# Optimization experiments

Hardware: AMD Instinct MI355X
Metric: run time of the kernel (lower is better)

The kernel has to match this reference:

```python
import jax, jax.numpy as jnp
import numpy as np

N, E, C, H, G = 100000, 1600000, 128, 64, 512
TOL = 1e-7          # PyG topk tolerance
MIN_SCORE = 0.05
EPS_KL = 1e-14


def setup_inputs() -> dict:
    key = jax.random.key(0)
    ks = jax.random.split(key, 12)
    d = {}
    d["x"] = jax.random.normal(ks[0], (N, C), jnp.float32)
    d["edge_index"] = jax.random.randint(ks[1], (2, E), 0, N)
    d["batch"] = jnp.sort(jax.random.randint(ks[2], (N,), 0, G))
    d["attn"] = jax.random.uniform(ks[3], (N,), jnp.float32, minval=1e-3, maxval=1.0)
    def lin(k, i, o):
        return (jax.random.normal(k, (i, o), jnp.float32) / np.sqrt(i)).astype(jnp.float32)
    d["W1"] = lin(ks[4], C, H); d["b1"] = jnp.zeros((H,), jnp.float32)
    d["W2"] = lin(ks[5], H, H); d["b2"] = jnp.zeros((H,), jnp.float32)
    d["pool_w"] = (jax.random.normal(ks[6], (C,), jnp.float32) / np.sqrt(C)).astype(jnp.float32)
    d["W3"] = lin(ks[7], H, H); d["b3"] = jnp.zeros((H,), jnp.float32)
    d["W4"] = lin(ks[8], H, H); d["b4"] = jnp.zeros((H,), jnp.float32)
    d["Wl"] = lin(ks[9], H, 1); d["bl"] = jnp.zeros((1,), jnp.float32)
    return d


def _gin(x, src, dst, Wa, ba, Wb, bb, edge_w=None):
    # GINConv with eps=0: nn((1+0)*x + sum_{j in N(i)} x_j), nn = Lin-ReLU-Lin
    msg = x[src]                                   # [E, F] gather
    if edge_w is not None:
        msg = msg * edge_w[:, None]                # drop pruned edges
    agg = jax.ops.segment_sum(msg, dst, num_segments=x.shape[0])
    h = x + agg
    return jax.nn.relu(h @ Wa + ba) @ Wb + bb


def reference(x, edge_index, batch, attn, W1, b1, W2, b2, pool_w, W3, b3, W4, b4, Wl, bl):
    src, dst = edge_index[0], edge_index[1]
    out = jax.nn.relu(_gin(x, src, dst, W1, b1, W2, b2))

    # --- TopKPooling(min_score=0.05), attn=x ---
    raw = x @ pool_w                               # [N] attention logits
    m = jax.ops.segment_max(raw, batch, num_segments=G)
    e = jnp.exp(raw - m[batch])
    z = jax.ops.segment_sum(e, batch, num_segments=G)
    score = e / z[batch]                           # per-graph softmax
    smax = jax.ops.segment_max(score, batch, num_segments=G)
    thresh = jnp.minimum(smax[batch] - TOL, MIN_SCORE)
    mask = score > thresh                          # kept nodes (>=1 per graph)
    maskf = mask.astype(x.dtype)
    out = out * (score * maskf)[:, None]           # x[perm] * score[perm]
    edge_keep = maskf[src] * maskf[dst]            # filter_adj: both endpoints kept

    out = jax.nn.relu(_gin(out, src, dst, W3, b3, W4, b4, edge_w=edge_keep)) * maskf[:, None]
    graph_out = jax.ops.segment_sum(out, batch, num_segments=G)  # global_add_pool
    pred = (graph_out @ Wl + bl).reshape(-1)       # [G]

    # attn_loss = scatter_mean(kl_div(log(score+eps), attn[perm]), batch)
    kl = attn * (jnp.log(attn) - jnp.log(score + EPS_KL))
    cnt = jax.ops.segment_sum(maskf, batch, num_segments=G)
    attn_loss = jax.ops.segment_sum(kl * maskf, batch, num_segments=G) / jnp.maximum(cnt, 1.0)

    ratio = maskf.sum() / x.shape[0]
    return pred, attn_loss, ratio
```

## Files before the change

### kernel.cpp

```cpp
#include <hip/hip_runtime.h>
#include <math.h>

#define N_NODES 100000
#define N_EDGES 1600000
#define C_IN    128
#define H_DIM   64
#define G_GRAPHS 512
#define MAXG    4096
#define ELCAP   65536
#define KPG     32
#define NBITS   3136

__device__ __forceinline__ int lbound(const int* __restrict__ b, int val) {
    int lo = 0, hi = N_NODES;
    while (lo < hi) {
        int mid = (lo + hi) >> 1;
        if (b[mid] < val) lo = mid + 1; else hi = mid;
    }
    return lo;
}

__global__ void kpre(const float* __restrict__ x, const float* __restrict__ pool_w,
                     float* __restrict__ sc, unsigned int* __restrict__ zero_region) {
    int gid = blockIdx.x * blockDim.x + threadIdx.x;
    if (gid < NBITS + 1) zero_region[gid] = 0u;
    const int lane = threadIdx.x & 63;
    const int l32  = lane & 31;
    const int half = lane >> 5;
    const float4 pwv = ((const float4*)pool_w)[l32];
    const int wid = blockIdx.x * (blockDim.x >> 6) + (threadIdx.x >> 6);
    const int nw  = gridDim.x * (blockDim.x >> 6);
    for (int r0 = wid * 4; r0 < N_NODES; r0 += nw * 4) {
        int rowA = r0 + half;
        int rowB = r0 + 2 + half;
        float4 xa = ((const float4*)(x + (size_t)rowA * C_IN))[l32];
        float4 xb = ((const float4*)(x + (size_t)rowB * C_IN))[l32];
        float pa = xa.x * pwv.x + xa.y * pwv.y + xa.z * pwv.z + xa.w * pwv.w;
        float pb = xb.x * pwv.x + xb.y * pwv.y + xb.z * pwv.z + xb.w * pwv.w;
        #pragma unroll
        for (int m = 16; m > 0; m >>= 1) {
            pa += __shfl_xor(pa, m, 64);
            pb += __shfl_xor(pb, m, 64);
        }
        if (l32 == 0) { sc[rowA] = pa; sc[rowB] = pb; }
    }
}

__device__ __forceinline__ float blk_max(float v, float* red, int lane, int w) {
    #pragma unroll
    for (int m = 32; m > 0; m >>= 1) v = fmaxf(v, __shfl_xor(v, m, 64));
    if (lane == 0) red[w] = v;
    __syncthreads();
    float r = fmaxf(fmaxf(red[0], red[1]), fmaxf(red[2], red[3]));
    __syncthreads();
    return r;
}
__device__ __forceinline__ float blk_sum(float v, float* red, int lane, int w) {
    #pragma unroll
    for (int m = 32; m > 0; m >>= 1) v += __shfl_xor(v, m, 64);
    if (lane == 0) red[w] = v;
    __syncthreads();
    float r = (red[0] + red[1]) + (red[2] + red[3]);
    __syncthreads();
    return r;
}

__global__ void kA4(const int* __restrict__ batch, const float* __restrict__ attn,
                    float* __restrict__ sc, unsigned int* __restrict__ kept_bits,
                    int* __restrict__ klist, int* __restrict__ kcnt,
                    float* __restrict__ B, float* __restrict__ out) {
    __shared__ float buf[MAXG];
    __shared__ float red[4];
    __shared__ int   lst[KPG];
    __shared__ int   cntk;
    const int g = blockIdx.x;
    const int t = threadIdx.x;
    const int lane = t & 63;
    const int w = t >> 6;
    const int ns = lbound(batch, g);
    const int ne = lbound(batch, g + 1);
    const int cn = ne - ns;
    if (cn <= 0) {
        if (t == 0) { out[G_GRAPHS + g] = 0.f; kcnt[g] = 0; }
        return;
    }
    if (t == 0) cntk = 0;
    float lmax = -3.4e38f;
    for (int i = t; i < cn; i += 256) { float r = sc[ns + i]; buf[i] = r; lmax = fmaxf(lmax, r); }
    float m = blk_max(lmax, red, lane, w);
    float lsum = 0.f;
    for (int i = t; i < cn; i += 256) { float e = expf(buf[i] - m); buf[i] = e; lsum += e; }
    float z = blk_sum(lsum, red, lane, w);
    float thresh = fminf(1.f / z - 1e-7f, 0.05f);
    float klacc = 0.f;
    for (int i = t; i < cn; i += 256) {
        float s = buf[i] / z;
        if (s > thresh) {
            int n = ns + i;
            int p = atomicAdd(&cntk, 1);
            if (p < KPG) lst[p] = i;
            sc[n] = s;
            float a = attn[n];
            klacc += a * (logf(a) - logf(s + 1e-14f));
        }
    }
    float klsum = blk_sum(klacc, red, lane, w);
    int kct = cntk;
    int kc = kct < KPG ? kct : KPG;
    if (t == 0) {
        out[G_GRAPHS + g] = (kct > 0) ? klsum / (float)kct : 0.f;
        kcnt[g] = kc;
    }
    for (int i = t; i < kc; i += 256) {
        int n = ns + lst[i];
        klist[g * KPG + i] = n;
        atomicOr(&kept_bits[n >> 5], 1u << (n & 31));
    }
    for (int j = t; j < kc * H_DIM; j += 256)
        B[(size_t)(ns + lst[j >> 6]) * H_DIM + (j & 63)] = 0.f;
}

__device__ __forceinline__ void emit(bool hit, int s, int d, int* __restrict__ list,
                                     int cap, int* __restrict__ count, int lane) {
    unsigned long long bal = __ballot(hit);
    if (bal == 0ull) return;
    int leader = __ffsll((long long)bal) - 1;
    int cnt = __popcll(bal);
    int base = 0;
    if (lane == leader) base = atomicAdd(count, cnt);
    base = __shfl(base, leader, 64);
    if (hit) {
        int p = base + __popcll(bal & ((1ull << lane) - 1ull));
        if (p < cap) { list[p] = s; list[cap + p] = d; }
    }
}

__global__ void k5f2(const int* __restrict__ ei, const unsigned int* __restrict__ bits,
                     const float* __restrict__ x, const float* __restrict__ W1,
                     float* __restrict__ B, int* __restrict__ elsd,
                     int* __restrict__ elcount) {
    __shared__ float W1s[C_IN * H_DIM];
    __shared__ int ls[1024], ld[1024];
    __shared__ int c1;
    const int t = threadIdx.x;
    const int lane = t & 63;
    if (t == 0) c1 = 0;
    int t4 = blockIdx.x * 256 + t;
    bool valid = t4 < (N_EDGES / 4);
    int4 s4 = make_int4(0, 0, 0, 0), d4 = make_int4(0, 0, 0, 0);
    if (valid) {
        s4 = ((const int4*)ei)[t4];
        d4 = ((const int4*)(ei + N_EDGES))[t4];
    }
    __syncthreads();
    int sv[4] = {s4.x, s4.y, s4.z, s4.w};
    int dv[4] = {d4.x, d4.y, d4.z, d4.w};
    bool bk[4];
    #pragma unroll
    for (int q = 0; q < 4; ++q) {
        int ss = sv[q], dd = dv[q];
        bool kd = valid && (((bits[dd >> 5] >> (dd & 31)) & 1u) != 0u);
        bk[q] = kd && (((bits[ss >> 5] >> (ss & 31)) & 1u) != 0u);
        if (kd) { int p = atomicAdd(&c1, 1); ls[p] = ss; ld[p] = dd; }
    }
    #pragma unroll
    for (int q = 0; q < 4; ++q) emit(bk[q], sv[q], dv[q], elsd, ELCAP, elcount, lane);
    __syncthreads();
    const int nloc = c1;
    if (nloc == 0) return;
    for (int i = t; i < C_IN * H_DIM; i += 256) W1s[i] = W1[i];
    __syncthreads();
    const int w = t >> 6;
    for (int idx = w; idx < nloc; idx += 4) {
        int s = ls[idx];
        int d = ld[idx];
        const float4* xr = (const float4*)(x + (size_t)s * C_IN);
        float acc = 0.f;
        #pragma unroll 8
        for (int k4 = 0; k4 < C_IN / 4; ++k4) {
            float4 xv = xr[k4];
            acc = fmaf(xv.x, W1s[(4 * k4 + 0) * H_DIM + lane], acc);
            acc = fmaf(xv.y, W1s[(4 * k4 + 1) * H_DIM + lane], acc);
            acc = fmaf(xv.z, W1s[(4 * k4 + 2) * H_DIM + lane], acc);
            acc = fmaf(xv.w, W1s[(4 * k4 + 3) * H_DIM + lane], acc);
        }
        atomicAdd(&B[(size_t)d * H_DIM + lane], acc);
    }
}

__device__ __forceinline__ float computeA(int n, int lane,
                                          const float* __restrict__ x,
                                          const float* __restrict__ B,
                                          const float* __restrict__ sc,
                                          const float* __restrict__ W1, float b1l,
                                          const float* __restrict__ W2, float b2l,
                                          const float* __restrict__ W3) {
    const float4* xr = (const float4*)(x + (size_t)n * C_IN);
    float u = 0.f;
    #pragma unroll 8
    for (int k4 = 0; k4 < C_IN / 4; ++k4) {
        float4 xv = xr[k4];
        u = fmaf(xv.x, W1[(4 * k4 + 0) * H_DIM + lane], u);
        u = fmaf(xv.y, W1[(4 * k4 + 1) * H_DIM + lane], u);
        u = fmaf(xv.z, W1[(4 * k4 + 2) * H_DIM + lane], u);
        u = fmaf(xv.w, W1[(4 * k4 + 3) * H_DIM + lane], u);
    }
    float t1 = fmaxf(u + B[(size_t)n * H_DIM + lane] + b1l, 0.f);
    float o1 = b2l;
    #pragma unroll 8
    for (int k = 0; k < H_DIM; ++k) o1 = fmaf(__shfl(t1, k, 64), W2[k * H_DIM + lane], o1);
    o1 = fmaxf(o1, 0.f);
    float v = 0.f;
    #pragma unroll 8
    for (int k = 0; k < H_DIM; ++k) v = fmaf(__shfl(o1, k, 64), W3[k * H_DIM + lane], v);
    return v * sc[n];
}

__global__ void k8c(const int* __restrict__ klist, const int* __restrict__ kcnt,
                    const float* __restrict__ sc, const float* __restrict__ x,
                    const float* __restrict__ W1, const float* __restrict__ b1,
                    const float* __restrict__ W2, const float* __restrict__ b2,
                    const float* __restrict__ W3, const float* __restrict__ b3,
                    const float* __restrict__ W4, const float* __restrict__ b4,
                    const float* __restrict__ Wl, const float* __restrict__ bl,
                    const float* __restrict__ B, const int* __restrict__ elsd,
                    const int* __restrict__ elcount, float* __restrict__ out) {
    const int g = blockIdx.x;
    const int lane = threadIdx.x;
    const float b1l = b1[lane], b2l = b2[lane], b3l = b3[lane], b4l = b4[lane];
    const int kc = kcnt[g];
    int ec = *elcount; if (ec > ELCAP) ec = ELCAP;
    float gsum = 0.f;
    for (int i = 0; i < kc; ++i) {
        int n = __builtin_amdgcn_readfirstlane(klist[g * KPG + i]);
        float agg = 0.f;
        for (int base = 0; base < ec; base += 64) {
            int idx = base + lane;
            int dd = (idx < ec) ? elsd[ELCAP + idx] : -1;
            bool mtc = (dd == n);
            int ssl = mtc ? elsd[idx] : 0;
            unsigned long long bal = __ballot(mtc);
            while (bal) {
                int j = __ffsll((long long)bal) - 1;
                bal &= bal - 1;
                int s = __builtin_amdgcn_readfirstlane(__shfl(ssl, j, 64));
                agg += computeA(s, lane, x, B, sc, W1, b1l, W2, b2l, W3);
            }
        }
        float vA = computeA(n, lane, x, B, sc, W1, b1l, W2, b2l, W3);
        float t = fmaxf(vA + agg + b3l, 0.f);
        float o2 = b4l;
        #pragma unroll 8
        for (int k = 0; k < H_DIM; ++k) o2 = fmaf(__shfl(t, k, 64), W4[k * H_DIM + lane], o2);
        gsum += fmaxf(o2, 0.f);
    }
    float p = gsum * Wl[lane];
    #pragma unroll
    for (int m = 32; m > 0; m >>= 1) p += __shfl_xor(p, m, 64);
    if (lane == 0) out[g] = p + bl[0];
    if (g == 0) {
        int tot = 0;
        for (int i = lane; i < G_GRAPHS; i += 64) tot += kcnt[i];
        #pragma unroll
        for (int m = 32; m > 0; m >>= 1) tot += __shfl_xor(tot, m, 64);
        if (lane == 0) out[2 * G_GRAPHS] = (float)tot * (1.f / (float)N_NODES);
    }
}

extern "C" void kernel_launch(void* const* d_in, const int* in_sizes, int n_in,
                              void* d_out, int out_size, void* d_ws, size_t ws_size,
                              hipStream_t stream) {
    const float* x      = (const float*)d_in[0];
    const int*   ei     = (const int*)d_in[1];
    const int*   batch  = (const int*)d_in[2];
    const float* attn   = (const float*)d_in[3];
    const float* W1     = (const float*)d_in[4];
    const float* b1     = (const float*)d_in[5];
    const float* W2     = (const float*)d_in[6];
    const float* b2     = (const float*)d_in[7];
    const float* pool_w = (const float*)d_in[8];
    const float* W3     = (const float*)d_in[9];
    const float* b3     = (const float*)d_in[10];
    const float* W4     = (const float*)d_in[11];
    const float* b4     = (const float*)d_in[12];
    const float* Wl     = (const float*)d_in[13];
    const float* bl     = (const float*)d_in[14];
    float* out = (float*)d_out;

    float* B      = (float*)d_ws;
    float* sc     = B + (size_t)N_NODES * H_DIM;
    int*   klist  = (int*)(sc + N_NODES);
    int*   kcnt   = klist + G_GRAPHS * KPG;
    int*   elsd   = kcnt + G_GRAPHS;
    unsigned int* kept_bits = (unsigned int*)(elsd + 2 * ELCAP);
    int*          elcount   = (int*)(kept_bits + NBITS);

    kpre <<<2048, 256, 0, stream>>>(x, pool_w, sc, kept_bits);
    kA4  <<<G_GRAPHS, 256, 0, stream>>>(batch, attn, sc, kept_bits, klist, kcnt, B, out);
    k5f2 <<<(N_EDGES / 4 + 255) / 256, 256, 0, stream>>>(ei, kept_bits, x, W1, B,
                                                         elsd, elcount);
    k8c  <<<G_GRAPHS, 64, 0, stream>>>(klist, kcnt, sc, x, W1, b1, W2, b2, W3, b3,
                                       W4, b4, Wl, bl, B, elsd, elcount, out);
}
```

Baseline: 172.5 us.

## Precompute per-node first-GIN output once and precompute graph offsets

The final kernel used to recompute the first GIN layer output for every in-edge source, once per destination node, and it rescanned the edge list once per kept node. This change adds a kernel that computes that output once per kept node and stores it in B. The final kernel then scans the edge list a single time per graph, matching destinations against the kept list and accumulating into shared memory. Graph start offsets are now built in the pre-pass instead of by per-block binary search, and the W1 shared-memory staging in the edge-scan kernel is replaced by direct global reads. The cost is one extra kernel launch and an overwrite of B that depends on kAcomp running after kscan.

```diff
diff --git a/kernel.cpp b/kernel.cpp
--- a/kernel.cpp
+++ b/kernel.cpp
@@ -11,19 +11,22 @@
 #define KPG     32
 #define NBITS   3136
 
-__device__ __forceinline__ int lbound(const int* __restrict__ b, int val) {
-    int lo = 0, hi = N_NODES;
-    while (lo < hi) {
-        int mid = (lo + hi) >> 1;
-        if (b[mid] < val) lo = mid + 1; else hi = mid;
-    }
-    return lo;
-}
-
 __global__ void kpre(const float* __restrict__ x, const float* __restrict__ pool_w,
-                     float* __restrict__ sc, unsigned int* __restrict__ zero_region) {
+                     const int* __restrict__ batch,
+                     float* __restrict__ sc, unsigned int* __restrict__ zero_region,
+                     int* __restrict__ gstart) {
     int gid = blockIdx.x * blockDim.x + threadIdx.x;
+    int nthr = gridDim.x * blockDim.x;
     if (gid < NBITS + 1) zero_region[gid] = 0u;
+    for (int i = gid; i < N_NODES; i += nthr) {
+        int b = batch[i];
+        int prev = (i == 0) ? -1 : batch[i - 1];
+        for (int g = prev + 1; g <= b; ++g) gstart[g] = i;
+    }
+    if (gid == 0) {
+        int last = batch[N_NODES - 1];
+        for (int g = last + 1; g <= G_GRAPHS; ++g) gstart[g] = N_NODES;
+    }
     const int lane = threadIdx.x & 63;
     const int l32  = lane & 31;
     const int half = lane >> 5;
@@ -65,7 +68,7 @@
     return r;
 }
 
-__global__ void kA4(const int* __restrict__ batch, const float* __restrict__ attn,
+__global__ void kA4(const int* __restrict__ gstart, const float* __restrict__ attn,
                     float* __restrict__ sc, unsigned int* __restrict__ kept_bits,
                     int* __restrict__ klist, int* __restrict__ kcnt,
                     float* __restrict__ B, float* __restrict__ out) {
@@ -77,8 +80,8 @@
     const int t = threadIdx.x;
     const int lane = t & 63;
     const int w = t >> 6;
-    const int ns = lbound(batch, g);
-    const int ne = lbound(batch, g + 1);
+    const int ns = gstart[g];
+    const int ne = gstart[g + 1];
     const int cn = ne - ns;
     if (cn <= 0) {
         if (t == 0) { out[G_GRAPHS + g] = 0.f; kcnt[g] = 0; }
@@ -135,11 +138,10 @@
     }
 }
 
-__global__ void k5f2(const int* __restrict__ ei, const unsigned int* __restrict__ bits,
-                     const float* __restrict__ x, const float* __restrict__ W1,
-                     float* __restrict__ B, int* __restrict__ elsd,
-                     int* __restrict__ elcount) {
-    __shared__ float W1s[C_IN * H_DIM];
+__global__ void kscan(const int* __restrict__ ei, const unsigned int* __restrict__ bits,
+                      const float* __restrict__ x, const float* __restrict__ W1,
+                      float* __restrict__ B, int* __restrict__ elsd,
+                      int* __restrict__ elcount) {
     __shared__ int ls[1024], ld[1024];
     __shared__ int c1;
     const int t = threadIdx.x;
@@ -168,8 +170,6 @@
     __syncthreads();
     const int nloc = c1;
     if (nloc == 0) return;
-    for (int i = t; i < C_IN * H_DIM; i += 256) W1s[i] = W1[i];
-    __syncthreads();
     const int w = t >> 6;
     for (int idx = w; idx < nloc; idx += 4) {
         int s = ls[idx];
@@ -179,10 +179,10 @@
         #pragma unroll 8
         for (int k4 = 0; k4 < C_IN / 4; ++k4) {
             float4 xv = xr[k4];
-            acc = fmaf(xv.x, W1s[(4 * k4 + 0) * H_DIM + lane], acc);
-            acc = fmaf(xv.y, W1s[(4 * k4 + 1) * H_DIM + lane], acc);
-            acc = fmaf(xv.z, W1s[(4 * k4 + 2) * H_DIM + lane], acc);
-            acc = fmaf(xv.w, W1s[(4 * k4 + 3) * H_DIM + lane], acc);
+            acc = fmaf(xv.x, W1[(4 * k4 + 0) * H_DIM + lane], acc);
+            acc = fmaf(xv.y, W1[(4 * k4 + 1) * H_DIM + lane], acc);
+            acc = fmaf(xv.z, W1[(4 * k4 + 2) * H_DIM + lane], acc);
+            acc = fmaf(xv.w, W1[(4 * k4 + 3) * H_DIM + lane], acc);
         }
         atomicAdd(&B[(size_t)d * H_DIM + lane], acc);
     }
@@ -216,39 +216,61 @@
     return v * sc[n];
 }
 
-__global__ void k8c(const int* __restrict__ klist, const int* __restrict__ kcnt,
-                    const float* __restrict__ sc, const float* __restrict__ x,
-                    const float* __restrict__ W1, const float* __restrict__ b1,
-                    const float* __restrict__ W2, const float* __restrict__ b2,
-                    const float* __restrict__ W3, const float* __restrict__ b3,
-                    const float* __restrict__ W4, const float* __restrict__ b4,
-                    const float* __restrict__ Wl, const float* __restrict__ bl,
-                    const float* __restrict__ B, const int* __restrict__ elsd,
+__global__ void kAcomp(const int* __restrict__ klist, const int* __restrict__ kcnt,
+                       const float* __restrict__ sc, const float* __restrict__ x,
+                       const float* __restrict__ W1, const float* __restrict__ b1,
+                       const float* __restrict__ W2, const float* __restrict__ b2,
+                       const float* __restrict__ W3, float* __restrict__ B) {
+    const int lane = threadIdx.x & 63;
+    const float b1l = b1[lane], b2l = b2[lane];
+    const int gw = blockIdx.x * (blockDim.x >> 6) + (threadIdx.x >> 6);
+    const int nw = gridDim.x * (blockDim.x >> 6);
+    for (int sl = gw; sl < G_GRAPHS * KPG; sl += nw) {
+        const int i = sl >> 9;
+        const int g = sl & (G_GRAPHS - 1);
+        if (i < kcnt[g]) {
+            int n = __builtin_amdgcn_readfirstlane(klist[g * KPG + i]);
+            float a = computeA(n, lane, x, B, sc, W1, b1l, W2, b2l, W3);
+            B[(size_t)n * H_DIM + lane] = a;
+        }
+    }
+}
+
+__global__ void k8f(const int* __restrict__ klist, const int* __restrict__ kcnt,
+                    const float* __restrict__ B,
+                    const float* __restrict__ b3, const float* __restrict__ W4,
+                    const float* __restrict__ b4, const float* __restrict__ Wl,
+                    const float* __restrict__ bl, const int* __restrict__ elsd,
                     const int* __restrict__ elcount, float* __restrict__ out) {
+    __shared__ float agg[KPG][H_DIM];
+    __shared__ int kl_s[KPG];
     const int g = blockIdx.x;
     const int lane = threadIdx.x;
-    const float b1l = b1[lane], b2l = b2[lane], b3l = b3[lane], b4l = b4[lane];
+    const float b3l = b3[lane], b4l = b4[lane];
     const int kc = kcnt[g];
+    if (lane < kc) kl_s[lane] = klist[g * KPG + lane];
+    for (int i = 0; i < kc; ++i) agg[i][lane] = 0.f;
+    __syncthreads();
     int ec = *elcount; if (ec > ELCAP) ec = ELCAP;
+    for (int base = 0; base < ec; base += 64) {
+        int idx = base + lane;
+        int d = (idx < ec) ? elsd[ELCAP + idx] : -1;
+        int pos = -1;
+        for (int i = 0; i < kc; ++i) if (kl_s[i] == d) pos = i;
+        int s = (pos >= 0) ? elsd[idx] : 0;
+        unsigned long long bal = __ballot(pos >= 0);
+        while (bal) {
+            int j = __ffsll((long long)bal) - 1;
+            bal &= bal - 1;
+            int su = __builtin_amdgcn_readfirstlane(__shfl(s, j, 64));
+            int pu = __builtin_amdgcn_readfirstlane(__shfl(pos, j, 64));
+            agg[pu][lane] += B[(size_t)su * H_DIM + lane];
+        }
+    }
     float gsum = 0.f;
     for (int i = 0; i < kc; ++i) {
-        int n = __builtin_amdgcn_readfirstlane(klist[g * KPG + i]);
-        float agg = 0.f;
-        for (int base = 0; base < ec; base += 64) {
-            int idx = base + lane;
-            int dd = (idx < ec) ? elsd[ELCAP + idx] : -1;
-            bool mtc = (dd == n);
-            int ssl = mtc ? elsd[idx] : 0;
-            unsigned long long bal = __ballot(mtc);
-            while (bal) {
-                int j = __ffsll((long long)bal) - 1;
-                bal &= bal - 1;
-                int s = __builtin_amdgcn_readfirstlane(__shfl(ssl, j, 64));
-                agg += computeA(s, lane, x, B, sc, W1, b1l, W2, b2l, W3);
-            }
-        }
-        float vA = computeA(n, lane, x, B, sc, W1, b1l, W2, b2l, W3);
-        float t = fmaxf(vA + agg + b3l, 0.f);
+        int n = __builtin_amdgcn_readfirstlane(kl_s[i]);
+        float t = fmaxf(B[(size_t)n * H_DIM + lane] + agg[i][lane] + b3l, 0.f);
         float o2 = b4l;
         #pragma unroll 8
         for (int k = 0; k < H_DIM; ++k) o2 = fmaf(__shfl(t, k, 64), W4[k * H_DIM + lane], o2);
@@ -294,11 +316,13 @@
     int*   elsd   = kcnt + G_GRAPHS;
     unsigned int* kept_bits = (unsigned int*)(elsd + 2 * ELCAP);
     int*          elcount   = (int*)(kept_bits + NBITS);
-
-    kpre <<<2048, 256, 0, stream>>>(x, pool_w, sc, kept_bits);
-    kA4  <<<G_GRAPHS, 256, 0, stream>>>(batch, attn, sc, kept_bits, klist, kcnt, B, out);
-    k5f2 <<<(N_EDGES / 4 + 255) / 256, 256, 0, stream>>>(ei, kept_bits, x, W1, B,
-                                                         elsd, elcount);
-    k8c  <<<G_GRAPHS, 64, 0, stream>>>(klist, kcnt, sc, x, W1, b1, W2, b2, W3, b3,
-                                       W4, b4, Wl, bl, B, elsd, elcount, out);
-}
+    int*          gstart    = elcount + 1;
+
+    kpre  <<<2048, 256, 0, stream>>>(x, pool_w, batch, sc, kept_bits, gstart);
+    kA4   <<<G_GRAPHS, 256, 0, stream>>>(gstart, attn, sc, kept_bits, klist, kcnt, B, out);
+    kscan <<<(N_EDGES / 4 + 255) / 256, 256, 0, stream>>>(ei, kept_bits, x, W1, B,
+                                                          elsd, elcount);
+    kAcomp<<<512, 256, 0, stream>>>(klist, kcnt, sc, x, W1, b1, W2, b2, W3, B);
+    k8f   <<<G_GRAPHS, 64, 0, stream>>>(klist, kcnt, B, b3, W4, b4, Wl, bl,
+                                        elsd, elcount, out);
+}
```

New measurement: 167.0 us. 1.03x faster.

## Fuse four kernels into one cooperative persistent kernel with grid syncs

Applied to the files above, without the earlier changes.

Replaces the four separate launches (score projection, per-graph softmax/top-k, edge filtering with the first-layer scatter, final MLP) with one cooperative kernel of one block per graph, separated by grid.sync. Graph boundaries now come from a parallel scan of the sorted batch array instead of per-block binary searches. The pool projection is computed per graph directly into shared memory. The final stage spreads kept nodes across four waves before a single-wave MLP. The aim is to cut launch gaps and extra global round trips. In exchange it adds grid-wide barriers, reads W1 from global memory instead of shared memory in the edge stage, and runs only 512 blocks across all phases.

```diff
diff --git a/kernel.cpp b/kernel.cpp
--- a/kernel.cpp
+++ b/kernel.cpp
@@ -1,5 +1,8 @@
 #include <hip/hip_runtime.h>
+#include <hip/hip_cooperative_groups.h>
 #include <math.h>
+
+namespace cg = cooperative_groups;
 
 #define N_NODES 100000
 #define N_EDGES 1600000
@@ -11,41 +14,6 @@
 #define KPG     32
 #define NBITS   3136
 
-__device__ __forceinline__ int lbound(const int* __restrict__ b, int val) {
-    int lo = 0, hi = N_NODES;
-    while (lo < hi) {
-        int mid = (lo + hi) >> 1;
-        if (b[mid] < val) lo = mid + 1; else hi = mid;
-    }
-    return lo;
-}
-
-__global__ void kpre(const float* __restrict__ x, const float* __restrict__ pool_w,
-                     float* __restrict__ sc, unsigned int* __restrict__ zero_region) {
-    int gid = blockIdx.x * blockDim.x + threadIdx.x;
-    if (gid < NBITS + 1) zero_region[gid] = 0u;
-    const int lane = threadIdx.x & 63;
-    const int l32  = lane & 31;
-    const int half = lane >> 5;
-    const float4 pwv = ((const float4*)pool_w)[l32];
-    const int wid = blockIdx.x * (blockDim.x >> 6) + (threadIdx.x >> 6);
-    const int nw  = gridDim.x * (blockDim.x >> 6);
-    for (int r0 = wid * 4; r0 < N_NODES; r0 += nw * 4) {
-        int rowA = r0 + half;
-        int rowB = r0 + 2 + half;
-        float4 xa = ((const float4*)(x + (size_t)rowA * C_IN))[l32];
-        float4 xb = ((const float4*)(x + (size_t)rowB * C_IN))[l32];
-        float pa = xa.x * pwv.x + xa.y * pwv.y + xa.z * pwv.z + xa.w * pwv.w;
-        float pb = xb.x * pwv.x + xb.y * pwv.y + xb.z * pwv.z + xb.w * pwv.w;
-        #pragma unroll
-        for (int m = 16; m > 0; m >>= 1) {
-            pa += __shfl_xor(pa, m, 64);
-            pb += __shfl_xor(pb, m, 64);
-        }
-        if (l32 == 0) { sc[rowA] = pa; sc[rowB] = pb; }
-    }
-}
-
 __device__ __forceinline__ float blk_max(float v, float* red, int lane, int w) {
     #pragma unroll
     for (int m = 32; m > 0; m >>= 1) v = fmaxf(v, __shfl_xor(v, m, 64));
@@ -63,61 +31,6 @@
     float r = (red[0] + red[1]) + (red[2] + red[3]);
     __syncthreads();
     return r;
-}
-
-__global__ void kA4(const int* __restrict__ batch, const float* __restrict__ attn,
-                    float* __restrict__ sc, unsigned int* __restrict__ kept_bits,
-                    int* __restrict__ klist, int* __restrict__ kcnt,
-                    float* __restrict__ B, float* __restrict__ out) {
-    __shared__ float buf[MAXG];
-    __shared__ float red[4];
-    __shared__ int   lst[KPG];
-    __shared__ int   cntk;
-    const int g = blockIdx.x;
-    const int t = threadIdx.x;
-    const int lane = t & 63;
-    const int w = t >> 6;
-    const int ns = lbound(batch, g);
-    const int ne = lbound(batch, g + 1);
-    const int cn = ne - ns;
-    if (cn <= 0) {
-        if (t == 0) { out[G_GRAPHS + g] = 0.f; kcnt[g] = 0; }
-        return;
-    }
-    if (t == 0) cntk = 0;
-    float lmax = -3.4e38f;
-    for (int i = t; i < cn; i += 256) { float r = sc[ns + i]; buf[i] = r; lmax = fmaxf(lmax, r); }
-    float m = blk_max(lmax, red, lane, w);
-    float lsum = 0.f;
-    for (int i = t; i < cn; i += 256) { float e = expf(buf[i] - m); buf[i] = e; lsum += e; }
-    float z = blk_sum(lsum, red, lane, w);
-    float thresh = fminf(1.f / z - 1e-7f, 0.05f);
-    float klacc = 0.f;
-    for (int i = t; i < cn; i += 256) {
-        float s = buf[i] / z;
-        if (s > thresh) {
-            int n = ns + i;
-            int p = atomicAdd(&cntk, 1);
-            if (p < KPG) lst[p] = i;
-            sc[n] = s;
-            float a = attn[n];
-            klacc += a * (logf(a) - logf(s + 1e-14f));
-        }
-    }
-    float klsum = blk_sum(klacc, red, lane, w);
-    int kct = cntk;
-    int kc = kct < KPG ? kct : KPG;
-    if (t == 0) {
-        out[G_GRAPHS + g] = (kct > 0) ? klsum / (float)kct : 0.f;
-        kcnt[g] = kc;
-    }
-    for (int i = t; i < kc; i += 256) {
-        int n = ns + lst[i];
-        klist[g * KPG + i] = n;
-        atomicOr(&kept_bits[n >> 5], 1u << (n & 31));
-    }
-    for (int j = t; j < kc * H_DIM; j += 256)
-        B[(size_t)(ns + lst[j >> 6]) * H_DIM + (j & 63)] = 0.f;
 }
 
 __device__ __forceinline__ void emit(bool hit, int s, int d, int* __restrict__ list,
@@ -132,59 +45,6 @@
     if (hit) {
         int p = base + __popcll(bal & ((1ull << lane) - 1ull));
         if (p < cap) { list[p] = s; list[cap + p] = d; }
-    }
-}
-
-__global__ void k5f2(const int* __restrict__ ei, const unsigned int* __restrict__ bits,
-                     const float* __restrict__ x, const float* __restrict__ W1,
-                     float* __restrict__ B, int* __restrict__ elsd,
-                     int* __restrict__ elcount) {
-    __shared__ float W1s[C_IN * H_DIM];
-    __shared__ int ls[1024], ld[1024];
-    __shared__ int c1;
-    const int t = threadIdx.x;
-    const int lane = t & 63;
-    if (t == 0) c1 = 0;
-    int t4 = blockIdx.x * 256 + t;
-    bool valid = t4 < (N_EDGES / 4);
-    int4 s4 = make_int4(0, 0, 0, 0), d4 = make_int4(0, 0, 0, 0);
-    if (valid) {
-        s4 = ((const int4*)ei)[t4];
-        d4 = ((const int4*)(ei + N_EDGES))[t4];
-    }
-    __syncthreads();
-    int sv[4] = {s4.x, s4.y, s4.z, s4.w};
-    int dv[4] = {d4.x, d4.y, d4.z, d4.w};
-    bool bk[4];
-    #pragma unroll
-    for (int q = 0; q < 4; ++q) {
-        int ss = sv[q], dd = dv[q];
-        bool kd = valid && (((bits[dd >> 5] >> (dd & 31)) & 1u) != 0u);
-        bk[q] = kd && (((bits[ss >> 5] >> (ss & 31)) & 1u) != 0u);
-        if (kd) { int p = atomicAdd(&c1, 1); ls[p] = ss; ld[p] = dd; }
-    }
-    #pragma unroll
-    for (int q = 0; q < 4; ++q) emit(bk[q], sv[q], dv[q], elsd, ELCAP, elcount, lane);
-    __syncthreads();
-    const int nloc = c1;
-    if (nloc == 0) return;
-    for (int i = t; i < C_IN * H_DIM; i += 256) W1s[i] = W1[i];
-    __syncthreads();
-    const int w = t >> 6;
-    for (int idx = w; idx < nloc; idx += 4) {
-        int s = ls[idx];
-        int d = ld[idx];
-        const float4* xr = (const float4*)(x + (size_t)s * C_IN);
-        float acc = 0.f;
-        #pragma unroll 8
-        for (int k4 = 0; k4 < C_IN / 4; ++k4) {
-            float4 xv = xr[k4];
-            acc = fmaf(xv.x, W1s[(4 * k4 + 0) * H_DIM + lane], acc);
-            acc = fmaf(xv.y, W1s[(4 * k4 + 1) * H_DIM + lane], acc);
-            acc = fmaf(xv.z, W1s[(4 * k4 + 2) * H_DIM + lane], acc);
-            acc = fmaf(xv.w, W1s[(4 * k4 + 3) * H_DIM + lane], acc);
-        }
-        atomicAdd(&B[(size_t)d * H_DIM + lane], acc);
     }
 }
 
@@ -216,23 +76,171 @@
     return v * sc[n];
 }
 
-__global__ void k8c(const int* __restrict__ klist, const int* __restrict__ kcnt,
-                    const float* __restrict__ sc, const float* __restrict__ x,
-                    const float* __restrict__ W1, const float* __restrict__ b1,
-                    const float* __restrict__ W2, const float* __restrict__ b2,
-                    const float* __restrict__ W3, const float* __restrict__ b3,
-                    const float* __restrict__ W4, const float* __restrict__ b4,
-                    const float* __restrict__ Wl, const float* __restrict__ bl,
-                    const float* __restrict__ B, const int* __restrict__ elsd,
-                    const int* __restrict__ elcount, float* __restrict__ out) {
+__global__ __launch_bounds__(256, 2) void mega(
+    const float* __restrict__ x, const int* __restrict__ ei,
+    const int* __restrict__ batch, const float* __restrict__ attn,
+    const float* __restrict__ W1, const float* __restrict__ b1,
+    const float* __restrict__ W2, const float* __restrict__ b2,
+    const float* __restrict__ pool_w,
+    const float* __restrict__ W3, const float* __restrict__ b3,
+    const float* __restrict__ W4, const float* __restrict__ b4,
+    const float* __restrict__ Wl, const float* __restrict__ bl,
+    float* __restrict__ B, float* __restrict__ sc,
+    int* __restrict__ klist, int* __restrict__ kcnt,
+    int* __restrict__ elsd, unsigned int* __restrict__ kept_bits,
+    int* __restrict__ elcount, int* __restrict__ gstart,
+    float* __restrict__ out)
+{
+    __shared__ float buf[MAXG];
+    __shared__ float red[4];
+    __shared__ int   lst[KPG];
+    __shared__ int   cntk;
+    __shared__ int   ls[1024], ld[1024];
+
+    cg::grid_group grid = cg::this_grid();
     const int g = blockIdx.x;
-    const int lane = threadIdx.x;
-    const float b1l = b1[lane], b2l = b2[lane], b3l = b3[lane], b4l = b4[lane];
-    const int kc = kcnt[g];
+    const int t = threadIdx.x;
+    const int lane = t & 63;
+    const int w = t >> 6;
+    const int gtid = g * 256 + t;
+    const int nthr = G_GRAPHS * 256;
+
+    if (gtid < NBITS + 1) kept_bits[gtid] = 0u;
+    for (int i = gtid; i < N_NODES; i += nthr) {
+        int b = batch[i];
+        int prev = (i == 0) ? -1 : batch[i - 1];
+        for (int gg = prev + 1; gg <= b; ++gg) gstart[gg] = i;
+    }
+    if (gtid == 0) {
+        int last = batch[N_NODES - 1];
+        for (int gg = last + 1; gg <= G_GRAPHS; ++gg) gstart[gg] = N_NODES;
+    }
+    grid.sync();
+
+    const int ns = gstart[g];
+    const int ne = gstart[g + 1];
+    const int cn = ne - ns;
+    const float b1l = b1[lane], b2l = b2[lane];
+    if (t == 0) cntk = 0;
+    int kc = 0;
+    if (cn > 0) {
+        const int l32  = lane & 31;
+        const int half = lane >> 5;
+        const float4 pwv = ((const float4*)pool_w)[l32];
+        for (int r0 = ns + w * 4; r0 < ne; r0 += 16) {
+            int rowA = r0 + half;
+            int rowB = r0 + 2 + half;
+            bool vA = rowA < ne, vB = rowB < ne;
+            float4 xa, xb;
+            if (vA) xa = ((const float4*)(x + (size_t)rowA * C_IN))[l32];
+            if (vB) xb = ((const float4*)(x + (size_t)rowB * C_IN))[l32];
+            if (vA) {
+                float pa = xa.x * pwv.x + xa.y * pwv.y + xa.z * pwv.z + xa.w * pwv.w;
+                #pragma unroll
+                for (int m = 16; m > 0; m >>= 1) pa += __shfl_xor(pa, m, 64);
+                if (l32 == 0) buf[rowA - ns] = pa;
+            }
+            if (vB) {
+                float pb = xb.x * pwv.x + xb.y * pwv.y + xb.z * pwv.z + xb.w * pwv.w;
+                #pragma unroll
+                for (int m = 16; m > 0; m >>= 1) pb += __shfl_xor(pb, m, 64);
+                if (l32 == 0) buf[rowB - ns] = pb;
+            }
+        }
+    }
+    __syncthreads();
+    if (cn > 0) {
+        float lmax = -3.4e38f;
+        for (int i = t; i < cn; i += 256) lmax = fmaxf(lmax, buf[i]);
+        float m = blk_max(lmax, red, lane, w);
+        float lsum = 0.f;
+        for (int i = t; i < cn; i += 256) { float e = expf(buf[i] - m); buf[i] = e; lsum += e; }
+        float z = blk_sum(lsum, red, lane, w);
+        float thresh = fminf(1.f / z - 1e-7f, 0.05f);
+        float klacc = 0.f;
+        for (int i = t; i < cn; i += 256) {
+            float s = buf[i] / z;
+            if (s > thresh) {
+                int n = ns + i;
+                int p = atomicAdd(&cntk, 1);
+                if (p < KPG) lst[p] = i;
+                sc[n] = s;
+                float a = attn[n];
+                klacc += a * (logf(a) - logf(s + 1e-14f));
+            }
+        }
+        float klsum = blk_sum(klacc, red, lane, w);
+        int kct = cntk;
+        kc = kct < KPG ? kct : KPG;
+        if (t == 0) {
+            out[G_GRAPHS + g] = (kct > 0) ? klsum / (float)kct : 0.f;
+            kcnt[g] = kc;
+        }
+        for (int i = t; i < kc; i += 256) {
+            int n = ns + lst[i];
+            klist[g * KPG + i] = n;
+            atomicOr(&kept_bits[n >> 5], 1u << (n & 31));
+        }
+        for (int j = t; j < kc * H_DIM; j += 256)
+            B[(size_t)(ns + lst[j >> 6]) * H_DIM + (j & 63)] = 0.f;
+    } else {
+        if (t == 0) { out[G_GRAPHS + g] = 0.f; kcnt[g] = 0; }
+    }
+    grid.sync();
+
+    const int NQ = N_EDGES / 4;
+    if (t == 0) cntk = 0;
+    __syncthreads();
+    #pragma unroll 1
+    for (int it = 0; it < (NQ + nthr - 1) / nthr; ++it) {
+        int t4 = it * nthr + gtid;
+        bool valid = t4 < NQ;
+        int4 s4 = make_int4(0, 0, 0, 0), d4 = make_int4(0, 0, 0, 0);
+        if (valid) {
+            s4 = ((const int4*)ei)[t4];
+            d4 = ((const int4*)(ei + N_EDGES))[t4];
+        }
+        int sv[4] = {s4.x, s4.y, s4.z, s4.w};
+        int dv[4] = {d4.x, d4.y, d4.z, d4.w};
+        bool bk[4];
+        #pragma unroll
+        for (int q = 0; q < 4; ++q) {
+            int ss = sv[q], dd = dv[q];
+            bool kd = valid && (((kept_bits[dd >> 5] >> (dd & 31)) & 1u) != 0u);
+            bk[q] = kd && (((kept_bits[ss >> 5] >> (ss & 31)) & 1u) != 0u);
+            if (kd) { int p = atomicAdd(&cntk, 1); ls[p] = ss; ld[p] = dd; }
+        }
+        #pragma unroll
+        for (int q = 0; q < 4; ++q) emit(bk[q], sv[q], dv[q], elsd, ELCAP, elcount, lane);
+        __syncthreads();
+        const int nloc = cntk;
+        for (int idx = w; idx < nloc; idx += 4) {
+            int s = ls[idx];
+            int d = ld[idx];
+            const float4* xr = (const float4*)(x + (size_t)s * C_IN);
+            float acc = 0.f;
+            #pragma unroll 8
+            for (int k4 = 0; k4 < C_IN / 4; ++k4) {
+                float4 xv = xr[k4];
+                acc = fmaf(xv.x, W1[(4 * k4 + 0) * H_DIM + lane], acc);
+                acc = fmaf(xv.y, W1[(4 * k4 + 1) * H_DIM + lane], acc);
+                acc = fmaf(xv.z, W1[(4 * k4 + 2) * H_DIM + lane], acc);
+                acc = fmaf(xv.w, W1[(4 * k4 + 3) * H_DIM + lane], acc);
+            }
+            atomicAdd(&B[(size_t)d * H_DIM + lane], acc);
+        }
+        __syncthreads();
+        if (t == 0) cntk = 0;
+        __syncthreads();
+    }
+    grid.sync();
+
+    float (*Abuf)[H_DIM] = (float(*)[H_DIM])buf;
+    float (*Gbuf)[H_DIM] = (float(*)[H_DIM])(buf + KPG * H_DIM);
     int ec = *elcount; if (ec > ELCAP) ec = ELCAP;
-    float gsum = 0.f;
-    for (int i = 0; i < kc; ++i) {
+    for (int i = w; i < kc; i += 4) {
         int n = __builtin_amdgcn_readfirstlane(klist[g * KPG + i]);
+        float vA = computeA(n, lane, x, B, sc, W1, b1l, W2, b2l, W3);
         float agg = 0.f;
         for (int base = 0; base < ec; base += 64) {
             int idx = base + lane;
@@ -247,22 +255,31 @@
                 agg += computeA(s, lane, x, B, sc, W1, b1l, W2, b2l, W3);
             }
         }
-        float vA = computeA(n, lane, x, B, sc, W1, b1l, W2, b2l, W3);
-        float t = fmaxf(vA + agg + b3l, 0.f);
-        float o2 = b4l;
-        #pragma unroll 8
-        for (int k = 0; k < H_DIM; ++k) o2 = fmaf(__shfl(t, k, 64), W4[k * H_DIM + lane], o2);
-        gsum += fmaxf(o2, 0.f);
-    }
-    float p = gsum * Wl[lane];
-    #pragma unroll
-    for (int m = 32; m > 0; m >>= 1) p += __shfl_xor(p, m, 64);
-    if (lane == 0) out[g] = p + bl[0];
-    if (g == 0) {
+        Abuf[i][lane] = vA;
+        Gbuf[i][lane] = agg;
+    }
+    __syncthreads();
+    if (w == 0) {
+        const float b3l = b3[lane], b4l = b4[lane];
+        float gsum = 0.f;
+        for (int i = 0; i < kc; ++i) {
+            float tt = fmaxf(Abuf[i][lane] + Gbuf[i][lane] + b3l, 0.f);
+            float o2 = b4l;
+            #pragma unroll 8
+            for (int k = 0; k < H_DIM; ++k)
+                o2 = fmaf(__shfl(tt, k, 64), W4[k * H_DIM + lane], o2);
+            gsum += fmaxf(o2, 0.f);
+        }
+        float p = gsum * Wl[lane];
+        #pragma unroll
+        for (int mm = 32; mm > 0; mm >>= 1) p += __shfl_xor(p, mm, 64);
+        if (lane == 0) out[g] = p + bl[0];
+    }
+    if (g == 0 && w == 1) {
         int tot = 0;
         for (int i = lane; i < G_GRAPHS; i += 64) tot += kcnt[i];
         #pragma unroll
-        for (int m = 32; m > 0; m >>= 1) tot += __shfl_xor(tot, m, 64);
+        for (int mm = 32; mm > 0; mm >>= 1) tot += __shfl_xor(tot, mm, 64);
         if (lane == 0) out[2 * G_GRAPHS] = (float)tot * (1.f / (float)N_NODES);
     }
 }
@@ -294,11 +311,15 @@
     int*   elsd   = kcnt + G_GRAPHS;
     unsigned int* kept_bits = (unsigned int*)(elsd + 2 * ELCAP);
     int*          elcount   = (int*)(kept_bits + NBITS);
-
-    kpre <<<2048, 256, 0, stream>>>(x, pool_w, sc, kept_bits);
-    kA4  <<<G_GRAPHS, 256, 0, stream>>>(batch, attn, sc, kept_bits, klist, kcnt, B, out);
-    k5f2 <<<(N_EDGES / 4 + 255) / 256, 256, 0, stream>>>(ei, kept_bits, x, W1, B,
-                                                         elsd, elcount);
-    k8c  <<<G_GRAPHS, 64, 0, stream>>>(klist, kcnt, sc, x, W1, b1, W2, b2, W3, b3,
-                                       W4, b4, Wl, bl, B, elsd, elcount, out);
-}
+    int*          gstart    = elcount + 1;
+
+    void* args[] = { (void*)&x, (void*)&ei, (void*)&batch, (void*)&attn,
+                     (void*)&W1, (void*)&b1, (void*)&W2, (void*)&b2,
+                     (void*)&pool_w, (void*)&W3, (void*)&b3, (void*)&W4,
+                     (void*)&b4, (void*)&Wl, (void*)&bl,
+                     (void*)&B, (void*)&sc, (void*)&klist, (void*)&kcnt,
+                     (void*)&elsd, (void*)&kept_bits, (void*)&elcount,
+                     (void*)&gstart, (void*)&out };
+    hipLaunchCooperativeKernel((const void*)mega, dim3(G_GRAPHS), dim3(256),
+                               args, 0, stream);
+}
```

After: 356.2 us. 2.06x slower.
